# Performance work log

Measured on AMD Instinct MI355X. Metric: run time of the kernel, lower is better.

The kernel has to match this reference:

```python
import jax, jax.numpy as jnp
import numpy as np

# Model dims (from init_kwargs)
I_N = 512          # input nodes
R_N = 16384        # reservoir nodes
N = I_N + R_N      # total nodes
BITS = 64          # input bits per step
CHUNKS = 2
B = BITS // CHUNKS # bits per chunk
K = 8              # k_max (max in-degree)
LUT_SIZE = 2 ** K
M = 64             # batch (parallel samples)
S = 16             # sequential steps
TICKS = (2, 2)     # reservoir ticks after each chunk perturbation ('22')
N_OUT = 10


def setup_inputs() -> dict:
    key = jax.random.key(0)
    ks = jax.random.split(key, 8)
    # input bit stream [m, s, c, b]
    x = jax.random.randint(ks[0], (M, S, CHUNKS, B), 0, 2).astype(jnp.float32)
    # sparse bipartite bit->input-node mapping [bits, I_N]
    w_in = jax.random.bernoulli(ks[1], 0.05, (BITS, I_N)).astype(jnp.float32)
    # homogenized incoming adjacency list [N, K] + validity mask (degree >= 1)
    deg = jax.random.randint(ks[2], (N,), 1, K + 1)
    adj_list = jax.random.randint(ks[3], (N, K), 0, N)
    adj_mask = (jnp.arange(K)[None, :] < deg[:, None])
    # random boolean lookup table [N, 2^K], p=0.5
    lut = jax.random.bernoulli(ks[4], 0.5, (N, LUT_SIZE)).astype(jnp.float32)
    # big-endian powers of two [K]
    powers_of_2 = 2.0 ** jnp.arange(K - 1, -1, -1, dtype=jnp.float32)
    initial_states = jax.random.bernoulli(ks[5], 0.5, (N,)).astype(jnp.float32)
    # readout Linear(R_N -> N_OUT)
    W_out = (jax.random.normal(ks[6], (N_OUT, R_N), dtype=jnp.float32)
             / np.sqrt(R_N).astype(np.float32))
    b_out = jnp.zeros((N_OUT,), jnp.float32)
    return dict(x=x, w_in=w_in, adj_list=adj_list, adj_mask=adj_mask, deg=deg,
                lut=lut, powers_of_2=powers_of_2, initial_states=initial_states,
                W_out=W_out, b_out=b_out)


def reference(x, w_in, adj_list, adj_mask, deg, lut, powers_of_2,
              initial_states, W_out, b_out):
    m = x.shape[0]
    node_ids = jnp.arange(N)
    maskf = adj_mask.astype(lut.dtype)        # [N, K]
    has_nb = (deg > 0)[None, :]               # nodes with no neighbours keep state

    def tick(states):
        # gather neighbour boolean states through the adjacency list: [m, N, K]
        neigh = states[:, adj_list] * maskf[None]
        # bin2int: pack K neighbour bits into a LUT index
        idx = jnp.einsum('mnk,k->mn', neigh, powers_of_2).astype(jnp.int32)
        new = lut[node_ids[None, :], idx]      # per-node LUT lookup [m, N]
        return jnp.where(has_nb, new, states)

    def step(states, x_s):  # x_s: [m, CHUNKS, B]
        for c in range(CHUNKS):
            w_c = w_in[c * B:(c + 1) * B]          # per-chunk slice of w_in
            inj = jnp.mod(x_s[:, c] @ w_c, 2.0)    # XOR-fold mapped bits [m, I_N]
            states = states.at[:, :I_N].set(jnp.mod(states[:, :I_N] + inj, 2.0))
            for _ in range(TICKS[c]):
                states = tick(states)
        return states, None

    states0 = jnp.tile(initial_states[None, :], (m, 1))   # [m, N]
    states, _ = jax.lax.scan(step, states0, jnp.swapaxes(x, 0, 1))
    # readout on reservoir (non-input) nodes, sigmoid activation
    out = states[:, I_N:] @ W_out.T + b_out
    return jax.nn.sigmoid(out)
```

## Files before the change

kernel.cpp:

```cpp
#include <hip/hip_runtime.h>

namespace {
constexpr int I_N   = 512;
constexpr int R_N   = 16384;
constexpr int NTOT  = 16896;
constexpr int ZW    = NTOT;
constexpr int N_OUT = 10;
constexpr int G     = 248;
constexpr int T     = 1024;
constexpr int NCH   = NTOT / 64;

constexpr size_t OFF_ADJ = 0;
constexpr size_t OFF_LUT = 540672;
constexpr size_t OFF_WPK = OFF_LUT + 540672;
constexpr size_t OFF_XPK = OFF_WPK + 4096;
constexpr size_t OFF_INJ = OFF_XPK + 8192;
constexpr size_t OFF_BAR = OFF_INJ + 131072;
constexpr size_t OFF_ST  = OFF_BAR + 65536;

using u64 = unsigned long long;
using u8  = unsigned char;

constexpr int PA_BIG = NTOT * 8;
constexpr int PA_W   = PA_BIG;
constexpr int PA_X   = PA_W + 1024;
constexpr int PA_B   = PA_X + 2048;
constexpr int PA_S   = PA_B + 9216;
constexpr int PA_TOT = PA_S + 32768;
}

__device__ __forceinline__ unsigned afa_sys(unsigned* p) {
  return __hip_atomic_fetch_add(p, 1u, __ATOMIC_RELAXED, __HIP_MEMORY_SCOPE_SYSTEM);
}
__device__ __forceinline__ unsigned lda_sys(const unsigned* p) {
  return __hip_atomic_load(p, __ATOMIC_RELAXED, __HIP_MEMORY_SCOPE_SYSTEM);
}
__device__ __forceinline__ void sta_sys(unsigned* p, unsigned v) {
  __hip_atomic_store(p, v, __ATOMIC_RELAXED, __HIP_MEMORY_SCOPE_SYSTEM);
}
__device__ __forceinline__ unsigned ld_l2(const unsigned* p) {
  return __hip_atomic_load(p, __ATOMIC_RELAXED, __HIP_MEMORY_SCOPE_AGENT);
}
__device__ __forceinline__ void st_l2(unsigned* p, unsigned v) {
  __hip_atomic_store(p, v, __ATOMIC_RELAXED, __HIP_MEMORY_SCOPE_AGENT);
}
__device__ __forceinline__ uint4 ld16_sc0(const void* p) {
  uint4 v;
  asm volatile("global_load_dwordx4 %0, %1, off sc0\n\ts_waitcnt vmcnt(0)"
               : "=v"(v) : "v"(p) : "memory");
  return v;
}
__device__ __forceinline__ u64 flipDiag(u64 x) {
  u64 t;
  t = 0x0f0f0f0f00000000ull & (x ^ (x << 28)); x ^= t ^ (t >> 28);
  t = 0x3333000033330000ull & (x ^ (x << 14)); x ^= t ^ (t >> 14);
  t = 0x5500550055005500ull & (x ^ (x << 7));  x ^= t ^ (t >> 7);
  return x;
}

__global__ __launch_bounds__(256) void prep_all(
    const int* __restrict__ adj, const int* __restrict__ deg,
    const float* __restrict__ lut, const float* __restrict__ x,
    const float* __restrict__ w_in, const float* __restrict__ init,
    unsigned* __restrict__ adjenc, unsigned* __restrict__ lutpk,
    unsigned* __restrict__ wpk, unsigned* __restrict__ xpk2,
    unsigned* __restrict__ bar, u8* __restrict__ st)
{
  int gid = blockIdx.x * 256 + threadIdx.x;
  if (gid < PA_BIG) {
    int n = gid >> 3, w = gid & 7;
    adjenc[gid] = (w < deg[n]) ? (unsigned)adj[gid] : (unsigned)ZW;
    const float* row = lut + (size_t)n * 256;
    unsigned word = 0;
    for (int i = 0; i < 32; ++i) {
      unsigned r = __brev((unsigned)(w * 32 + i)) >> 24;
      word |= (row[r] > 0.5f ? 1u : 0u) << i;
    }
    lutpk[gid] = word;
  } else if (gid < PA_X) {
    int i2 = gid - PA_W;
    int c = i2 >> 9, i = i2 & 511;
    unsigned w = 0;
    for (int b = 0; b < 32; ++b)
      w |= (w_in[(c * 32 + b) * 512 + i] > 0.5f ? 1u : 0u) << b;
    wpk[i2] = w;
  } else if (gid < PA_B) {
    int j = gid - PA_X;
    const float* xp = x + (size_t)j * 32;
    unsigned w = 0;
    for (int b = 0; b < 32; ++b) w |= (xp[b] > 0.5f ? 1u : 0u) << b;
    xpk2[(j & 31) * 64 + (j >> 5)] = w;
  } else if (gid < PA_S) {
    bar[gid - PA_B] = 0u;
  } else {
    int j = gid - PA_S;
    int g = j >> 12, i = j & 4095;
    int n = I_N + i * 4;
    unsigned v = 0;
    #pragma unroll
    for (int b = 0; b < 4; ++b)
      v |= (init[n + b] > 0.5f ? 0xFFu : 0x00u) << (8 * b);
    *(unsigned*)(st + (size_t)g * NTOT + n) = v;
  }
}

__global__ __launch_bounds__(256) void inj_pack(
    const unsigned* __restrict__ wpk, const unsigned* __restrict__ xpk2,
    const float* __restrict__ init, u8* __restrict__ inj8, u8* __restrict__ st)
{
  int gid = blockIdx.x * 256 + threadIdx.x;
  int g = gid >> 14, sc = (gid >> 9) & 31, n = gid & 511;
  int c = sc & 1;
  unsigned wb = wpk[c * 512 + n];
  unsigned acc = 0;
  #pragma unroll
  for (int b = 0; b < 8; ++b) {
    unsigned xw = xpk2[sc * 64 + g * 8 + b];
    acc |= (unsigned)(__popc(xw & wb) & 1) << b;
  }
  inj8[gid] = (u8)acc;
  if (sc == 0)
    st[(size_t)g * NTOT + n] = (u8)(((init[n] > 0.5f) ? 0xFFu : 0x00u) ^ acc);
}

__global__ __launch_bounds__(1024) void reservoir_main(
    const unsigned* __restrict__ adjenc, const unsigned* __restrict__ lutpk,
    const u8* __restrict__ inj8, u8* __restrict__ st, unsigned* __restrict__ bar)
{
  extern __shared__ char dynpad[];
  (void)dynpad;
  __shared__ __align__(16) u8 sstate[16960];
  __shared__ unsigned lutlds[9216];
  __shared__ int s_grp, s_slot, s_cnt;
  const int tid = threadIdx.x;
  const int lane = tid & 63;

  if (tid == 0) {
    unsigned xcc;
    asm volatile("s_getreg_b32 %0, hwreg(HW_REG_XCC_ID)" : "=s"(xcc));
    int g = (int)(xcc & 7u);
    s_grp = g;
    s_slot = (int)afa_sys(&bar[32 + g * 16]);
    asm volatile("s_waitcnt vmcnt(0)" ::: "memory");
    unsigned r = afa_sys(&bar[0]);
    if (r == (unsigned)(G - 1)) sta_sys(&bar[16], 1u);
    while (lda_sys(&bar[16]) < 1u) __builtin_amdgcn_s_sleep(2);
    s_cnt = (int)lda_sys(&bar[32 + g * 16]);
  }
  __syncthreads();
  const int g = s_grp;
  const unsigned kcnt = (unsigned)s_cnt;
  const int slot = s_slot;
  const unsigned wpg = kcnt * 16u;
  const unsigned wgid = (unsigned)slot * 16u + (unsigned)(tid >> 6);
  const unsigned clo = (wgid * (unsigned)NCH + wpg - 1u) / wpg;
  const unsigned chi = ((wgid + 1u) * (unsigned)NCH + wpg - 1u) / wpg;
  const bool hasC = clo < chi && clo < (unsigned)NCH;

  int n0 = 0; bool isInj0 = false;
  uint4 A0 = {0,0,0,0}, B0 = {0,0,0,0};
  if (hasC) {
    n0 = (int)(clo * 64u) + lane;
    const uint4* ap = reinterpret_cast<const uint4*>(adjenc + ((size_t)n0 << 3));
    A0 = ap[0]; B0 = ap[1];
    #pragma unroll
    for (int w = 0; w < 8; ++w)
      lutlds[tid * 9 + w] = lutpk[((size_t)n0 << 3) + w];
    isInj0 = n0 < I_N;
  }
  if (tid == 0) *(u64*)&sstate[16896] = 0ull;

  const unsigned sB = (((unsigned)(tid >> 2) * wpg) / (unsigned)NCH) >> 4;
  const unsigned sT = ((((256u + (unsigned)(tid >> 2))) * wpg / (unsigned)NCH)) >> 4;
  unsigned* flags = bar + 1024;
  const unsigned* fB = flags + ((unsigned)g * 64u + sB) * 16u;
  const unsigned* fT = flags + ((unsigned)g * 64u + sT) * 16u;
  unsigned* fMy = flags + ((unsigned)g * 64u + (unsigned)slot) * 16u;

  u8* gbase = st + (size_t)g * NTOT;

  for (int tt = 1; tt <= 64; ++tt) {
    const u8* src = gbase + (size_t)((tt - 1) & 3) * (8 * NTOT);
    u8*       dst = gbase + (size_t)(tt & 3) * (8 * NTOT);

    {
      unsigned need = (unsigned)(tt - 1);
      unsigned f;
      do { f = ld_l2(fB); } while (f < need);
      uint4 v = ld16_sc0(src + tid * 16);
      *reinterpret_cast<uint4*>(&sstate[tid * 16]) = v;
      if (tid < 32) {
        do { f = ld_l2(fT); } while (f < need);
        uint4 v2 = ld16_sc0(src + 16384 + tid * 16);
        *reinterpret_cast<uint4*>(&sstate[16384 + tid * 16]) = v2;
      }
    }
    __syncthreads();

    if (hasC) {
      unsigned b0 = sstate[A0.x], b1 = sstate[A0.y];
      unsigned b2 = sstate[A0.z], b3 = sstate[A0.w];
      unsigned b4 = sstate[B0.x], b5 = sstate[B0.y];
      unsigned b6 = sstate[B0.z], b7 = sstate[B0.w];
      unsigned lo = b0 | (b1 << 8) | (b2 << 16) | (b3 << 24);
      unsigned hi = b4 | (b5 << 8) | (b6 << 16) | (b7 << 24);
      u64 y = flipDiag(((u64)hi << 32) | lo);
      unsigned out = 0;
      #pragma unroll
      for (int j = 0; j < 8; ++j) {
        unsigned idx = (unsigned)(y >> (8 * j)) & 255u;
        unsigned w = lutlds[tid * 9 + (idx >> 5)];
        out |= ((w >> (idx & 31u)) & 1u) << j;
      }
      if (isInj0 && (tt & 1) == 0 && tt < 64)
        out ^= inj8[(size_t)(g * 32 + (tt >> 1)) * 512 + n0];
      dst[n0] = (u8)out;
      for (unsigned c = clo + 1; c < chi && c < (unsigned)NCH; ++c) {
        int n = (int)(c * 64u) + lane;
        const uint4* ap = reinterpret_cast<const uint4*>(adjenc + ((size_t)n << 3));
        uint4 A = ap[0], B = ap[1];
        unsigned d0 = sstate[A.x], d1 = sstate[A.y], d2 = sstate[A.z], d3 = sstate[A.w];
        unsigned d4 = sstate[B.x], d5 = sstate[B.y], d6 = sstate[B.z], d7 = sstate[B.w];
        unsigned l2 = d0 | (d1 << 8) | (d2 << 16) | (d3 << 24);
        unsigned h2 = d4 | (d5 << 8) | (d6 << 16) | (d7 << 24);
        u64 y2 = flipDiag(((u64)h2 << 32) | l2);
        unsigned o2 = 0;
        #pragma unroll
        for (int j = 0; j < 8; ++j) {
          unsigned idx = (unsigned)(y2 >> (8 * j)) & 255u;
          unsigned w = lutpk[((size_t)n << 3) + (idx >> 5)];
          o2 |= ((w >> (idx & 31u)) & 1u) << j;
        }
        if (n < I_N && (tt & 1) == 0 && tt < 64)
          o2 ^= inj8[(size_t)(g * 32 + (tt >> 1)) * 512 + n];
        dst[n] = (u8)o2;
      }
    }
    __syncthreads();
    if (tid == 0) st_l2(fMy, (unsigned)tt);
  }
}

__global__ __launch_bounds__(512) void readout_k(
    const u8* __restrict__ st, const float* __restrict__ Wout,
    const float* __restrict__ bout, float* __restrict__ out)
{
  const int m = blockIdx.x;
  const int gg = m >> 3, b = m & 7;
  const int lane = threadIdx.x & 63;
  const u8* sp = st + (size_t)gg * NTOT + I_N;
  float acc[N_OUT];
  #pragma unroll
  for (int o = 0; o < N_OUT; ++o) acc[o] = 0.f;
  for (int r = threadIdx.x; r < R_N; r += 512) {
    float bf = (float)((sp[r] >> b) & 1u);
    #pragma unroll
    for (int o = 0; o < N_OUT; ++o)
      acc[o] += bf * Wout[(size_t)o * R_N + r];
  }
  #pragma unroll
  for (int o = 0; o < N_OUT; ++o)
    for (int off = 32; off > 0; off >>= 1)
      acc[o] += __shfl_down(acc[o], off);
  __shared__ float red[8][N_OUT];
  if (lane == 0) {
    int w8 = threadIdx.x >> 6;
    #pragma unroll
    for (int o = 0; o < N_OUT; ++o) red[w8][o] = acc[o];
  }
  __syncthreads();
  if (threadIdx.x < N_OUT) {
    float v = bout[threadIdx.x];
    for (int w8 = 0; w8 < 8; ++w8) v += red[w8][threadIdx.x];
    out[m * N_OUT + threadIdx.x] = 1.0f / (1.0f + expf(-v));
  }
}

extern "C" void kernel_launch(void* const* d_in, const int* in_sizes, int n_in,
                              void* d_out, int out_size, void* d_ws, size_t ws_size,
                              hipStream_t stream)
{
  const float* x    = (const float*)d_in[0];
  const float* w_in = (const float*)d_in[1];
  const int*   adj  = (const int*)d_in[2];
  const int*   deg  = (const int*)d_in[4];
  const float* lut  = (const float*)d_in[5];
  const float* init = (const float*)d_in[7];
  const float* Wout = (const float*)d_in[8];
  const float* bout = (const float*)d_in[9];

  char* ws = (char*)d_ws;
  unsigned* adjenc = (unsigned*)(ws + OFF_ADJ);
  unsigned* lutpk  = (unsigned*)(ws + OFF_LUT);
  unsigned* wpk    = (unsigned*)(ws + OFF_WPK);
  unsigned* xpk2   = (unsigned*)(ws + OFF_XPK);
  u8*       inj8   = (u8*)(ws + OFF_INJ);
  unsigned* bar    = (unsigned*)(ws + OFF_BAR);
  u8*       st     = (u8*)(ws + OFF_ST);

  hipLaunchKernelGGL(prep_all, dim3(PA_TOT / 256), dim3(256), 0, stream,
                     adj, deg, lut, x, w_in, init, adjenc, lutpk, wpk, xpk2, bar, st);
  hipLaunchKernelGGL(inj_pack, dim3(512), dim3(256), 0, stream,
                     wpk, xpk2, init, inj8, st);
  hipLaunchKernelGGL(reservoir_main, dim3(G), dim3(T), 40960, stream,
                     adjenc, lutpk, inj8, st, bar);
  hipLaunchKernelGGL(readout_k, dim3(64), dim3(512), 0, stream,
                     st, Wout, bout, (float*)d_out);
}
```

Measured before the change: 197.1 us.

## Double-buffer LDS state mirror and prefetch next tick's state during compute

Replaces the single shared-memory state copy with two buffers. Idle waves, and waves that finish early, opportunistically poll peer flags and copy the next tick's state into the alternate buffer while other waves are still computing. A fallback wait-and-copy runs after the barrier. Flag layout is compacted from one flag per 64-byte line to contiguous words. Compute waves also raise their scheduling priority during the LDS gathers. The extra LDS use raises dynamic shared memory, which could hurt occupancy, and packing the flags together may add cache-line contention.

```diff
diff --git a/kernel.cpp b/kernel.cpp
--- a/kernel.cpp
+++ b/kernel.cpp
@@ -129,7 +129,7 @@
 {
   extern __shared__ char dynpad[];
   (void)dynpad;
-  __shared__ __align__(16) u8 sstate[16960];
+  __shared__ __align__(16) u8 mir[2][16960];
   __shared__ unsigned lutlds[9216];
   __shared__ int s_grp, s_slot, s_cnt;
   const int tid = threadIdx.x;
@@ -168,40 +168,37 @@
       lutlds[tid * 9 + w] = lutpk[((size_t)n0 << 3) + w];
     isInj0 = n0 < I_N;
   }
-  if (tid == 0) *(u64*)&sstate[16896] = 0ull;
-
-  const unsigned sB = (((unsigned)(tid >> 2) * wpg) / (unsigned)NCH) >> 4;
-  const unsigned sT = ((((256u + (unsigned)(tid >> 2))) * wpg / (unsigned)NCH)) >> 4;
+
   unsigned* flags = bar + 1024;
-  const unsigned* fB = flags + ((unsigned)g * 64u + sB) * 16u;
-  const unsigned* fT = flags + ((unsigned)g * 64u + sT) * 16u;
-  unsigned* fMy = flags + ((unsigned)g * 64u + (unsigned)slot) * 16u;
+  unsigned* fMy = flags + (unsigned)g * 64u + (unsigned)slot;
+  const unsigned c0u = (unsigned)tid >> 2;
+  const unsigned* f0 = flags + (unsigned)g * 64u + (((c0u * wpg) / (unsigned)NCH) >> 4);
+  const unsigned c1u = (1024u + (unsigned)tid) >> 2;
+  const unsigned* f1 = flags + (unsigned)g * 64u + (((c1u * wpg) / (unsigned)NCH) >> 4);
+  const bool hasU1 = tid < 32;
 
   u8* gbase = st + (size_t)g * NTOT;
 
+  *reinterpret_cast<uint4*>(&mir[0][tid * 16]) =
+      *reinterpret_cast<const uint4*>(gbase + tid * 16);
+  if (hasU1)
+    *reinterpret_cast<uint4*>(&mir[0][16384 + tid * 16]) =
+        *reinterpret_cast<const uint4*>(gbase + 16384 + tid * 16);
+  if (tid == 0) { *(u64*)&mir[0][16896] = 0ull; *(u64*)&mir[1][16896] = 0ull; }
+  __syncthreads();
+
+  int cur = 0;
   for (int tt = 1; tt <= 64; ++tt) {
-    const u8* src = gbase + (size_t)((tt - 1) & 3) * (8 * NTOT);
-    u8*       dst = gbase + (size_t)(tt & 3) * (8 * NTOT);
-
-    {
-      unsigned need = (unsigned)(tt - 1);
-      unsigned f;
-      do { f = ld_l2(fB); } while (f < need);
-      uint4 v = ld16_sc0(src + tid * 16);
-      *reinterpret_cast<uint4*>(&sstate[tid * 16]) = v;
-      if (tid < 32) {
-        do { f = ld_l2(fT); } while (f < need);
-        uint4 v2 = ld16_sc0(src + 16384 + tid * 16);
-        *reinterpret_cast<uint4*>(&sstate[16384 + tid * 16]) = v2;
-      }
-    }
-    __syncthreads();
+    u8* dst = gbase + (size_t)(tt & 3) * (8 * NTOT);
+    const u8* mb = mir[cur];
+    u8* mn = mir[cur ^ 1];
+    bool done0 = false, done1 = false;
+    const unsigned ttu = (unsigned)tt;
 
     if (hasC) {
-      unsigned b0 = sstate[A0.x], b1 = sstate[A0.y];
-      unsigned b2 = sstate[A0.z], b3 = sstate[A0.w];
-      unsigned b4 = sstate[B0.x], b5 = sstate[B0.y];
-      unsigned b6 = sstate[B0.z], b7 = sstate[B0.w];
+      __builtin_amdgcn_s_setprio(1);
+      unsigned b0 = mb[A0.x], b1 = mb[A0.y], b2 = mb[A0.z], b3 = mb[A0.w];
+      unsigned b4 = mb[B0.x], b5 = mb[B0.y], b6 = mb[B0.z], b7 = mb[B0.w];
       unsigned lo = b0 | (b1 << 8) | (b2 << 16) | (b3 << 24);
       unsigned hi = b4 | (b5 << 8) | (b6 << 16) | (b7 << 24);
       u64 y = flipDiag(((u64)hi << 32) | lo);
@@ -212,6 +209,7 @@
         unsigned w = lutlds[tid * 9 + (idx >> 5)];
         out |= ((w >> (idx & 31u)) & 1u) << j;
       }
+      __builtin_amdgcn_s_setprio(0);
       if (isInj0 && (tt & 1) == 0 && tt < 64)
         out ^= inj8[(size_t)(g * 32 + (tt >> 1)) * 512 + n0];
       dst[n0] = (u8)out;
@@ -219,8 +217,8 @@
         int n = (int)(c * 64u) + lane;
         const uint4* ap = reinterpret_cast<const uint4*>(adjenc + ((size_t)n << 3));
         uint4 A = ap[0], B = ap[1];
-        unsigned d0 = sstate[A.x], d1 = sstate[A.y], d2 = sstate[A.z], d3 = sstate[A.w];
-        unsigned d4 = sstate[B.x], d5 = sstate[B.y], d6 = sstate[B.z], d7 = sstate[B.w];
+        unsigned d0 = mb[A.x], d1 = mb[A.y], d2 = mb[A.z], d3 = mb[A.w];
+        unsigned d4 = mb[B.x], d5 = mb[B.y], d6 = mb[B.z], d7 = mb[B.w];
         unsigned l2 = d0 | (d1 << 8) | (d2 << 16) | (d3 << 24);
         unsigned h2 = d4 | (d5 << 8) | (d6 << 16) | (d7 << 24);
         u64 y2 = flipDiag(((u64)h2 << 32) | l2);
@@ -235,9 +233,36 @@
           o2 ^= inj8[(size_t)(g * 32 + (tt >> 1)) * 512 + n];
         dst[n] = (u8)o2;
       }
+    } else if (tt < 64) {
+      #pragma unroll
+      for (int rep = 0; rep < 2; ++rep) {
+        if (!done0 && ld_l2(f0) >= ttu) {
+          *reinterpret_cast<uint4*>(&mn[tid * 16]) = ld16_sc0(dst + tid * 16);
+          done0 = true;
+        }
+        if (hasU1 && !done1 && ld_l2(f1) >= ttu) {
+          *reinterpret_cast<uint4*>(&mn[16384 + tid * 16]) =
+              ld16_sc0(dst + 16384 + tid * 16);
+          done1 = true;
+        }
+      }
     }
     __syncthreads();
-    if (tid == 0) st_l2(fMy, (unsigned)tt);
+    if (tid == 0) st_l2(fMy, ttu);
+
+    if (tt < 64) {
+      if (!done0) {
+        unsigned f; do { f = ld_l2(f0); } while (f < ttu);
+        *reinterpret_cast<uint4*>(&mn[tid * 16]) = ld16_sc0(dst + tid * 16);
+      }
+      if (hasU1 && !done1) {
+        unsigned f; do { f = ld_l2(f1); } while (f < ttu);
+        *reinterpret_cast<uint4*>(&mn[16384 + tid * 16]) =
+            ld16_sc0(dst + 16384 + tid * 16);
+      }
+      __syncthreads();
+    }
+    cur ^= 1;
   }
 }
 
@@ -302,7 +327,7 @@
                      adj, deg, lut, x, w_in, init, adjenc, lutpk, wpk, xpk2, bar, st);
   hipLaunchKernelGGL(inj_pack, dim3(512), dim3(256), 0, stream,
                      wpk, xpk2, init, inj8, st);
-  hipLaunchKernelGGL(reservoir_main, dim3(G), dim3(T), 40960, stream,
+  hipLaunchKernelGGL(reservoir_main, dim3(G), dim3(T), 60000, stream,
                      adjenc, lutpk, inj8, st, bar);
   hipLaunchKernelGGL(readout_k, dim3(64), dim3(512), 0, stream,
                      st, Wout, bout, (float*)d_out);
```

Result: slower. 371.3 us (+88.4%).
